# Optimization experiments

Hardware: AMD Instinct MI355X
Metric: run time of the kernel (lower is better)

## Reference

```python
import jax, jax.numpy as jnp
import numpy as np

N_ROI = 262144
FEATURE_DIM = 256
HIDDEN_DIM = 64
N_NETWORKS = 128


def setup_inputs() -> dict:
    key = jax.random.key(0)
    ks = jax.random.split(key, 5)
    x = jax.random.normal(ks[0], (N_ROI, FEATURE_DIM), dtype=jnp.float32)
    group = jax.random.randint(ks[1], (N_ROI,), 0, N_NETWORKS, dtype=jnp.int32)
    W1 = jax.random.normal(ks[2], (FEATURE_DIM, HIDDEN_DIM), dtype=jnp.float32) / np.sqrt(FEATURE_DIM)
    b1 = jnp.zeros((HIDDEN_DIM,), dtype=jnp.float32)
    W2 = jax.random.normal(ks[3], (HIDDEN_DIM, 1), dtype=jnp.float32) / np.sqrt(HIDDEN_DIM)
    b2 = jnp.zeros((1,), dtype=jnp.float32)
    return {"x": x, "group": group, "W1": W1, "b1": b1, "W2": W2, "b2": b2}


def reference(x, group, W1, b1, W2, b2):
    # attention MLP score per ROI: Linear -> ReLU -> Linear(->1)
    h = jax.nn.relu(x @ W1 + b1)                       # [N, H]
    score = (h @ W2)[:, 0] + b2[0]                     # [N]
    # numerically-stable segment softmax over each network's ROIs
    seg_max = jax.ops.segment_max(score, group, num_segments=N_NETWORKS)  # [K]
    seg_max = jnp.where(jnp.isfinite(seg_max), seg_max, 0.0)              # empty segments -> 0
    w = jnp.exp(score - seg_max[group])                # [N] unnormalized weights
    denom = jax.ops.segment_sum(w, group, num_segments=N_NETWORKS)        # [K]
    num = jax.ops.segment_sum(w[:, None] * x, group, num_segments=N_NETWORKS)  # [K, D]
    # empty networks produce zeros (matches torch.zeros_like branch)
    return jnp.where(denom[:, None] > 0, num / jnp.maximum(denom, 1e-30)[:, None], 0.0)
```

## Files before the change

kernel.cpp:

```cpp
#include <hip/hip_runtime.h>
#include <hip/hip_bf16.h>

#define N_ROI 262144
#define FDIM  256
#define HDIM  64
#define NNET  128

#define CHUNK  64
#define NCHUNK 16
#define RPB    (CHUNK * NCHUNK)
#define NBLK   (N_ROI / RPB)
#define XPITCH 264
#define WPITCH 264
#define APITCH 72
#define STRIP  40.0f

typedef __attribute__((ext_vector_type(8))) __bf16 bf16x8;
typedef __attribute__((ext_vector_type(8))) short short8;
typedef __attribute__((ext_vector_type(4))) float floatx4;

union frag_cast { short8 s; bf16x8 b; };

#define NEG_INF (-__builtin_huge_valf())

__device__ __forceinline__ unsigned fkey(float f) {
  unsigned u = __float_as_uint(f);
  return (u & 0x80000000u) ? ~u : (u | 0x80000000u);
}
__device__ __forceinline__ float fkey_inv(unsigned k) {
  unsigned u = (k & 0x80000000u) ? (k ^ 0x80000000u) : ~k;
  return __uint_as_float(u);
}
__device__ __forceinline__ unsigned short f2bf(float f) {
  unsigned u = __float_as_uint(f);
  u += 0x7FFFu + ((u >> 16) & 1u);
  return (unsigned short)(u >> 16);
}
__device__ __forceinline__ float bf2f(unsigned short h) {
  return __uint_as_float(((unsigned)h) << 16);
}
__device__ __forceinline__ unsigned cvt2(float a, float b) {
  union { __hip_bfloat162 h; unsigned u; } cv;
  cv.h = __float22bfloat162_rn(make_float2(a, b));
  return cv.u;
}
__device__ __forceinline__ int sidx(int row, int s) {
  return row * XPITCH + (s ^ (((row >> 3) & 3) << 4));
}

__device__ __forceinline__ void block_bar() {
  __builtin_amdgcn_sched_barrier(0);
  asm volatile("s_waitcnt lgkmcnt(0)" ::: "memory");
  __builtin_amdgcn_s_barrier();
  __builtin_amdgcn_sched_barrier(0);
}

__global__ __launch_bounds__(1024, 4) void fused_kernel(
    const float* __restrict__ x, const int* __restrict__ group,
    const float* __restrict__ W1, const float* __restrict__ b1,
    const float* __restrict__ W2,
    float* __restrict__ num_ws,
    float* __restrict__ den_ws,
    float* __restrict__ m_ws)
{
  __shared__ __align__(16) unsigned short w1t[HDIM][WPITCH];
  __shared__ __align__(16) unsigned short xl[2][CHUNK * XPITCH];
  __shared__ __align__(16) unsigned short Alds[2][NNET * APITCH];
  __shared__ float scpart[4][CHUNK];
  __shared__ unsigned tmax[NNET];
  __shared__ __align__(16) float fl[NNET];
  __shared__ float mrunL[NNET];
  __shared__ float dent[2][NNET];
  __shared__ int sflag[2];

  const int tid  = threadIdx.x;
  const int wave = tid >> 6, lane = tid & 63;
  const int col  = lane & 15, quad = lane >> 4;
  const int h    = wave >> 2;
  const int mt   = wave & 3;
  const int bid  = blockIdx.x;
  const size_t rbase = (size_t)bid * RPB;

  {
    const int n = tid & 63, kg = tid >> 6;
#pragma unroll
    for (int p = 0; p < 2; ++p) {
      const int k0 = (p * 16 + kg) * 8;
      unsigned short tmp[8];
#pragma unroll
      for (int j = 0; j < 8; ++j) tmp[j] = f2bf(W1[(k0 + j) * HDIM + n]);
      *(short8*)&w1t[n][k0] = *(short8*)tmp;
    }
  }
  if (tid < NNET) { mrunL[tid] = 0.f; dent[1][tid] = 0.f; }
  if (tid == 0) sflag[1] = 0;
  float denrun = 0.f;

  const float b1s = b1[h * 16 + col];
  const float w2s = W2[h * 16 + col];

  floatx4 acc[8];
#pragma unroll
  for (int m2 = 0; m2 < 8; ++m2) acc[m2] = (floatx4)0.f;

  const float* xb = x + rbase * FDIM;
  const short8 zero8 = (short8)0;

  float4 pf[4];
#pragma unroll
  for (int i = 0; i < 4; ++i) pf[i] = *(const float4*)(xb + i * 4096 + tid * 4);
#pragma unroll
  for (int i = 0; i < 4; ++i) {
    const int row = i * 16 + wave;
    uint2 pk; pk.x = cvt2(pf[i].x, pf[i].y); pk.y = cvt2(pf[i].z, pf[i].w);
    *(uint2*)&xl[0][sidx(row, (tid & 63) * 4)] = pk;
  }
#pragma unroll
  for (int i = 0; i < 4; ++i)
    pf[i] = *(const float4*)(xb + 16384 + i * 4096 + tid * 4);
  block_bar();

  int gch = 0;
  for (int ch = 0; ch < NCHUNK; ++ch) {
    const int b = ch & 1;

    if (sflag[b ^ 1]) {
#pragma unroll
      for (int m2 = 0; m2 < 8; ++m2) {
        const floatx4 f4 = *(const floatx4*)&fl[m2 * 16 + quad * 4];
#pragma unroll
        for (int r = 0; r < 4; ++r) acc[m2][r] *= f4[r];
      }
      if (tid < NNET) denrun *= fl[tid];
    }
    if (tid < NNET) denrun += dent[b ^ 1][tid];

    if (tid < CHUNK) gch = group[rbase + ch * CHUNK + tid];
    for (int k8 = tid; k8 < (NNET * APITCH) / 8; k8 += 1024)
      *(short8*)&Alds[b][k8 * 8] = zero8;
    if (tid < NNET) { tmax[tid] = 0u; dent[b][tid] = 0.f; }
    if (tid == 0) sflag[b] = 0;

    floatx4 accS = (floatx4)0.f;
#pragma unroll
    for (int c = 0; c < 8; ++c) {
      frag_cast af, bw;
      af.s = *(const short8*)&xl[b][sidx(mt * 16 + col, c * 32 + quad * 8)];
      bw.s = *(const short8*)&w1t[h * 16 + col][c * 32 + quad * 8];
      accS = __builtin_amdgcn_mfma_f32_16x16x32_bf16(af.b, bw.b, accS, 0, 0, 0);
    }
    {
      float pr[4];
#pragma unroll
      for (int r = 0; r < 4; ++r) pr[r] = fmaxf(accS[r] + b1s, 0.f) * w2s;
#pragma unroll
      for (int off = 1; off < 16; off <<= 1)
#pragma unroll
        for (int r = 0; r < 4; ++r) pr[r] += __shfl_xor(pr[r], off, 16);
      if (col == 0) {
#pragma unroll
        for (int r = 0; r < 4; ++r) scpart[h][mt * 16 + quad * 4 + r] = pr[r];
      }
    }

    if (ch > 0) {
#pragma unroll
      for (int cc = 0; cc < 2; ++cc) {
        frag_cast bfx;
        {
          unsigned short bb[8];
#pragma unroll
          for (int j = 0; j < 8; ++j)
            bb[j] = xl[b ^ 1][sidx(cc * 32 + quad * 8 + j, wave * 16 + col)];
          bfx.s = *(short8*)bb;
        }
#pragma unroll
        for (int m2 = 0; m2 < 8; ++m2) {
          frag_cast af;
          af.s = *(const short8*)&Alds[b ^ 1][(m2 * 16 + col) * APITCH + cc * 32 + quad * 8];
          acc[m2] = __builtin_amdgcn_mfma_f32_16x16x32_bf16(af.b, bfx.b, acc[m2], 0, 0, 0);
        }
      }
    }
    block_bar();

    if (tid < CHUNK) {
      const float s = scpart[0][tid] + scpart[1][tid] + scpart[2][tid] + scpart[3][tid];
      const float m = mrunL[gch];
      const bool trip = !(s - m <= STRIP);
      const unsigned long long bal = __ballot(trip);
      if (bal == 0ull) {
        const float w = __expf(s - m);
        const unsigned short wb = f2bf(w);
        Alds[b][gch * APITCH + tid] = wb;
        atomicAdd(&dent[b][gch], bf2f(wb));
      } else {
        atomicMax(&tmax[gch], fkey(s));
        asm volatile("s_waitcnt lgkmcnt(0)" ::: "memory");
#pragma unroll
        for (int hh = 0; hh < 2; ++hh) {
          const int gi = tid + hh * 64;
          const unsigned tk = tmax[gi];
          float f = 1.f;
          float mo = mrunL[gi];
          if (tk) {
            const float mn = fmaxf(mo, fkey_inv(tk));
            f = __expf(mo - mn);
            mo = mn;
            mrunL[gi] = mn;
          }
          fl[gi] = f;
        }
        asm volatile("s_waitcnt lgkmcnt(0)" ::: "memory");
        {
          const float w = __expf(s - mrunL[gch]);
          const unsigned short wb = f2bf(w);
          Alds[b][gch * APITCH + tid] = wb;
          atomicAdd(&dent[b][gch], bf2f(wb));
        }
        if (tid == 0) sflag[b] = 1;
      }
    }
    if (ch < NCHUNK - 1) {
#pragma unroll
      for (int i = 0; i < 4; ++i) {
        const int row = i * 16 + wave;
        uint2 pk; pk.x = cvt2(pf[i].x, pf[i].y); pk.y = cvt2(pf[i].z, pf[i].w);
        *(uint2*)&xl[b ^ 1][sidx(row, (tid & 63) * 4)] = pk;
      }
      if (ch < NCHUNK - 2) {
#pragma unroll
        for (int i = 0; i < 4; ++i)
          pf[i] = *(const float4*)(xb + (size_t)(ch + 2) * 16384 + i * 4096 + tid * 4);
      }
    }
    block_bar();
  }

  {
    const int b = (NCHUNK - 1) & 1;
    if (sflag[b]) {
#pragma unroll
      for (int m2 = 0; m2 < 8; ++m2) {
        const floatx4 f4 = *(const floatx4*)&fl[m2 * 16 + quad * 4];
#pragma unroll
        for (int r = 0; r < 4; ++r) acc[m2][r] *= f4[r];
      }
      if (tid < NNET) denrun *= fl[tid];
    }
    if (tid < NNET) denrun += dent[b][tid];
#pragma unroll
    for (int cc = 0; cc < 2; ++cc) {
      frag_cast bfx;
      {
        unsigned short bb[8];
#pragma unroll
        for (int j = 0; j < 8; ++j)
          bb[j] = xl[b][sidx(cc * 32 + quad * 8 + j, wave * 16 + col)];
        bfx.s = *(short8*)bb;
      }
#pragma unroll
      for (int m2 = 0; m2 < 8; ++m2) {
        frag_cast af;
        af.s = *(const short8*)&Alds[b][(m2 * 16 + col) * APITCH + cc * 32 + quad * 8];
        acc[m2] = __builtin_amdgcn_mfma_f32_16x16x32_bf16(af.b, bfx.b, acc[m2], 0, 0, 0);
      }
    }
  }

#pragma unroll
  for (int m2 = 0; m2 < 8; ++m2)
#pragma unroll
    for (int r = 0; r < 4; ++r) {
      const int g = m2 * 16 + quad * 4 + r;
      num_ws[((size_t)g * NBLK + bid) * FDIM + wave * 16 + col] = acc[m2][r];
    }
  if (tid < NNET) {
    den_ws[(size_t)tid * NBLK + bid] = denrun;
    m_ws[(size_t)tid * NBLK + bid]   = mrunL[tid];
  }
}

__global__ __launch_bounds__(256) void finalize_kernel(
    const float* __restrict__ num_ws, const float* __restrict__ den_ws,
    const float* __restrict__ m_ws, float* __restrict__ out)
{
  const int g   = blockIdx.x;
  const int tid = threadIdx.x;
  __shared__ float e_l[NBLK];
  __shared__ float red[8];

  const float mb = m_ws[(size_t)g * NBLK + tid];
  float M = mb;
#pragma unroll
  for (int off = 1; off < 64; off <<= 1) M = fmaxf(M, __shfl_xor(M, off));
  if ((tid & 63) == 0) red[tid >> 6] = M;
  __syncthreads();
  M = fmaxf(fmaxf(red[0], red[1]), fmaxf(red[2], red[3]));

  const float eb = (mb == NEG_INF) ? 0.f : __expf(mb - M);
  e_l[tid] = eb;
  float dp = den_ws[(size_t)g * NBLK + tid] * eb;
#pragma unroll
  for (int off = 1; off < 64; off <<= 1) dp += __shfl_xor(dp, off);
  if ((tid & 63) == 0) red[4 + (tid >> 6)] = dp;
  __syncthreads();
  const float den = red[4] + red[5] + red[6] + red[7];

  float nsum = 0.f;
  const float* base = num_ws + (size_t)g * NBLK * FDIM + tid;
#pragma unroll 8
  for (int b = 0; b < NBLK; ++b)
    nsum += base[(size_t)b * FDIM] * e_l[b];
  out[g * FDIM + tid] = (den > 0.f) ? nsum / fmaxf(den, 1e-30f) : 0.f;
}

extern "C" void kernel_launch(void* const* d_in, const int* in_sizes, int n_in,
                              void* d_out, int out_size, void* d_ws, size_t ws_size,
                              hipStream_t stream)
{
  const float* x     = (const float*)d_in[0];
  const int*   group = (const int*)d_in[1];
  const float* W1    = (const float*)d_in[2];
  const float* b1    = (const float*)d_in[3];
  const float* W2    = (const float*)d_in[4];
  float* out = (float*)d_out;

  float* num_ws = (float*)d_ws;
  float* den_ws = num_ws + (size_t)NNET * NBLK * FDIM;
  float* m_ws   = den_ws + (size_t)NNET * NBLK;

  fused_kernel<<<NBLK, 1024, 0, stream>>>(x, group, W1, b1, W2, num_ws, den_ws, m_ws);
  finalize_kernel<<<NNET, 256, 0, stream>>>(num_ws, den_ws, m_ws, out);

  (void)in_sizes; (void)n_in; (void)out_size; (void)ws_size;
}
```

Measured before the change: 380.9 us.

## Specialize waves into score and scatter groups with single sparsely-cleared A buffer

Waves 0-7 now compute only the score GEMM, two row tiles each. Waves 8-15 own the weighted-scatter accumulation, two feature tiles each, with accumulators doubled per wave. The double-buffered one-hot weight matrix becomes a single buffer: instead of zeroing it every chunk, only the entries written in the previous chunk are cleared. An XOR swizzle is added to the W1 and weight-matrix LDS layouts to cut bank conflicts. The goal is to drop the full per-chunk LDS zeroing and to overlap the two GEMM phases across SIMDs. In exchange, the wave groups now carry unequal MFMA loads, and the scatter waves need more registers.

Result: slower. 440.6 us (+15.7%).

```diff
diff --git a/kernel.cpp b/kernel.cpp
--- a/kernel.cpp
+++ b/kernel.cpp
@@ -46,6 +46,9 @@
 }
 __device__ __forceinline__ int sidx(int row, int s) {
   return row * XPITCH + (s ^ (((row >> 3) & 3) << 4));
+}
+__device__ __forceinline__ int cswz(int row, int k) {
+  return k ^ ((row & 3) << 4);
 }
 
 __device__ __forceinline__ void block_bar() {
@@ -65,7 +68,7 @@
 {
   __shared__ __align__(16) unsigned short w1t[HDIM][WPITCH];
   __shared__ __align__(16) unsigned short xl[2][CHUNK * XPITCH];
-  __shared__ __align__(16) unsigned short Alds[2][NNET * APITCH];
+  __shared__ __align__(16) unsigned short Alds[NNET * APITCH];
   __shared__ float scpart[4][CHUNK];
   __shared__ unsigned tmax[NNET];
   __shared__ __align__(16) float fl[NNET];
@@ -76,8 +79,10 @@
   const int tid  = threadIdx.x;
   const int wave = tid >> 6, lane = tid & 63;
   const int col  = lane & 15, quad = lane >> 4;
-  const int h    = wave >> 2;
-  const int mt   = wave & 3;
+  const bool is_scat = (wave >= 8);
+  const int d8   = wave & 7;
+  const int h    = (wave >> 1) & 3;
+  const int mt0  = (wave & 1) * 2;
   const int bid  = blockIdx.x;
   const size_t rbase = (size_t)bid * RPB;
 
@@ -89,22 +94,24 @@
       unsigned short tmp[8];
 #pragma unroll
       for (int j = 0; j < 8; ++j) tmp[j] = f2bf(W1[(k0 + j) * HDIM + n]);
-      *(short8*)&w1t[n][k0] = *(short8*)tmp;
+      *(short8*)&w1t[n][cswz(n, k0)] = *(short8*)tmp;
     }
   }
   if (tid < NNET) { mrunL[tid] = 0.f; dent[1][tid] = 0.f; }
   if (tid == 0) sflag[1] = 0;
+  const short8 zero8 = (short8)0;
+  for (int k8 = tid; k8 < (NNET * APITCH) / 8; k8 += 1024)
+    *(short8*)&Alds[k8 * 8] = zero8;
   float denrun = 0.f;
 
   const float b1s = b1[h * 16 + col];
   const float w2s = W2[h * 16 + col];
 
-  floatx4 acc[8];
-#pragma unroll
-  for (int m2 = 0; m2 < 8; ++m2) acc[m2] = (floatx4)0.f;
+  floatx4 acc[8][2];
+#pragma unroll
+  for (int m2 = 0; m2 < 8; ++m2) { acc[m2][0] = (floatx4)0.f; acc[m2][1] = (floatx4)0.f; }
 
   const float* xb = x + rbase * FDIM;
-  const short8 zero8 = (short8)0;
 
   float4 pf[4];
 #pragma unroll
@@ -120,65 +127,76 @@
     pf[i] = *(const float4*)(xb + 16384 + i * 4096 + tid * 4);
   block_bar();
 
-  int gch = 0;
+  int gch = 0, gprev = 0;
   for (int ch = 0; ch < NCHUNK; ++ch) {
     const int b = ch & 1;
 
-    if (sflag[b ^ 1]) {
-#pragma unroll
-      for (int m2 = 0; m2 < 8; ++m2) {
-        const floatx4 f4 = *(const floatx4*)&fl[m2 * 16 + quad * 4];
-#pragma unroll
-        for (int r = 0; r < 4; ++r) acc[m2][r] *= f4[r];
-      }
-      if (tid < NNET) denrun *= fl[tid];
-    }
-    if (tid < NNET) denrun += dent[b ^ 1][tid];
-
+    if (tid < NNET) {
+      if (sflag[b ^ 1]) denrun *= fl[tid];
+      denrun += dent[b ^ 1][tid];
+      tmax[tid] = 0u; dent[b][tid] = 0.f;
+    }
+    if (tid == 0) sflag[b] = 0;
     if (tid < CHUNK) gch = group[rbase + ch * CHUNK + tid];
-    for (int k8 = tid; k8 < (NNET * APITCH) / 8; k8 += 1024)
-      *(short8*)&Alds[b][k8 * 8] = zero8;
-    if (tid < NNET) { tmax[tid] = 0u; dent[b][tid] = 0.f; }
-    if (tid == 0) sflag[b] = 0;
-
-    floatx4 accS = (floatx4)0.f;
-#pragma unroll
-    for (int c = 0; c < 8; ++c) {
-      frag_cast af, bw;
-      af.s = *(const short8*)&xl[b][sidx(mt * 16 + col, c * 32 + quad * 8)];
-      bw.s = *(const short8*)&w1t[h * 16 + col][c * 32 + quad * 8];
-      accS = __builtin_amdgcn_mfma_f32_16x16x32_bf16(af.b, bw.b, accS, 0, 0, 0);
-    }
-    {
-      float pr[4];
-#pragma unroll
-      for (int r = 0; r < 4; ++r) pr[r] = fmaxf(accS[r] + b1s, 0.f) * w2s;
-#pragma unroll
-      for (int off = 1; off < 16; off <<= 1)
-#pragma unroll
-        for (int r = 0; r < 4; ++r) pr[r] += __shfl_xor(pr[r], off, 16);
-      if (col == 0) {
-#pragma unroll
-        for (int r = 0; r < 4; ++r) scpart[h][mt * 16 + quad * 4 + r] = pr[r];
-      }
-    }
-
-    if (ch > 0) {
-#pragma unroll
-      for (int cc = 0; cc < 2; ++cc) {
-        frag_cast bfx;
-        {
-          unsigned short bb[8];
-#pragma unroll
-          for (int j = 0; j < 8; ++j)
-            bb[j] = xl[b ^ 1][sidx(cc * 32 + quad * 8 + j, wave * 16 + col)];
-          bfx.s = *(short8*)bb;
-        }
+
+    if (!is_scat) {
+      floatx4 accS[2];
+      accS[0] = (floatx4)0.f; accS[1] = (floatx4)0.f;
+#pragma unroll
+      for (int c = 0; c < 8; ++c) {
+        frag_cast bw;
+        bw.s = *(const short8*)&w1t[h * 16 + col][cswz(col, c * 32 + quad * 8)];
+#pragma unroll
+        for (int mtl = 0; mtl < 2; ++mtl) {
+          frag_cast af;
+          af.s = *(const short8*)&xl[b][sidx((mt0 + mtl) * 16 + col, c * 32 + quad * 8)];
+          accS[mtl] = __builtin_amdgcn_mfma_f32_16x16x32_bf16(af.b, bw.b, accS[mtl], 0, 0, 0);
+        }
+      }
+#pragma unroll
+      for (int mtl = 0; mtl < 2; ++mtl) {
+        float pr[4];
+#pragma unroll
+        for (int r = 0; r < 4; ++r) pr[r] = fmaxf(accS[mtl][r] + b1s, 0.f) * w2s;
+#pragma unroll
+        for (int off = 1; off < 16; off <<= 1)
+#pragma unroll
+          for (int r = 0; r < 4; ++r) pr[r] += __shfl_xor(pr[r], off, 16);
+        if (col == 0) {
+#pragma unroll
+          for (int r = 0; r < 4; ++r)
+            scpart[h][(mt0 + mtl) * 16 + quad * 4 + r] = pr[r];
+        }
+      }
+    } else {
+      if (sflag[b ^ 1]) {
 #pragma unroll
         for (int m2 = 0; m2 < 8; ++m2) {
-          frag_cast af;
-          af.s = *(const short8*)&Alds[b ^ 1][(m2 * 16 + col) * APITCH + cc * 32 + quad * 8];
-          acc[m2] = __builtin_amdgcn_mfma_f32_16x16x32_bf16(af.b, bfx.b, acc[m2], 0, 0, 0);
+          const floatx4 f4 = *(const floatx4*)&fl[m2 * 16 + quad * 4];
+#pragma unroll
+          for (int r = 0; r < 4; ++r) { acc[m2][0][r] *= f4[r]; acc[m2][1][r] *= f4[r]; }
+        }
+      }
+      if (ch > 0) {
+#pragma unroll
+        for (int cc = 0; cc < 2; ++cc) {
+          frag_cast bfx[2];
+#pragma unroll
+          for (int nt = 0; nt < 2; ++nt) {
+            unsigned short bb[8];
+#pragma unroll
+            for (int j = 0; j < 8; ++j)
+              bb[j] = xl[b ^ 1][sidx(cc * 32 + quad * 8 + j, d8 * 32 + nt * 16 + col)];
+            bfx[nt].s = *(short8*)bb;
+          }
+#pragma unroll
+          for (int m2 = 0; m2 < 8; ++m2) {
+            frag_cast af;
+            af.s = *(const short8*)&Alds[(m2 * 16 + col) * APITCH
+                                         + cswz(col, cc * 32 + quad * 8)];
+            acc[m2][0] = __builtin_amdgcn_mfma_f32_16x16x32_bf16(af.b, bfx[0].b, acc[m2][0], 0, 0, 0);
+            acc[m2][1] = __builtin_amdgcn_mfma_f32_16x16x32_bf16(af.b, bfx[1].b, acc[m2][1], 0, 0, 0);
+          }
         }
       }
     }
@@ -186,13 +204,14 @@
 
     if (tid < CHUNK) {
       const float s = scpart[0][tid] + scpart[1][tid] + scpart[2][tid] + scpart[3][tid];
+      Alds[gprev * APITCH + (tid ^ ((gprev & 3) << 4))] = 0;
       const float m = mrunL[gch];
       const bool trip = !(s - m <= STRIP);
       const unsigned long long bal = __ballot(trip);
       if (bal == 0ull) {
         const float w = __expf(s - m);
         const unsigned short wb = f2bf(w);
-        Alds[b][gch * APITCH + tid] = wb;
+        Alds[gch * APITCH + (tid ^ ((gch & 3) << 4))] = wb;
         atomicAdd(&dent[b][gch], bf2f(wb));
       } else {
         atomicMax(&tmax[gch], fkey(s));
@@ -202,11 +221,10 @@
           const int gi = tid + hh * 64;
           const unsigned tk = tmax[gi];
           float f = 1.f;
-          float mo = mrunL[gi];
           if (tk) {
+            const float mo = mrunL[gi];
             const float mn = fmaxf(mo, fkey_inv(tk));
             f = __expf(mo - mn);
-            mo = mn;
             mrunL[gi] = mn;
           }
           fl[gi] = f;
@@ -215,11 +233,12 @@
         {
           const float w = __expf(s - mrunL[gch]);
           const unsigned short wb = f2bf(w);
-          Alds[b][gch * APITCH + tid] = wb;
+          Alds[gch * APITCH + (tid ^ ((gch & 3) << 4))] = wb;
           atomicAdd(&dent[b][gch], bf2f(wb));
         }
         if (tid == 0) sflag[b] = 1;
       }
+      gprev = gch;
     }
     if (ch < NCHUNK - 1) {
 #pragma unroll
@@ -239,42 +258,53 @@
 
   {
     const int b = (NCHUNK - 1) & 1;
-    if (sflag[b]) {
-#pragma unroll
-      for (int m2 = 0; m2 < 8; ++m2) {
-        const floatx4 f4 = *(const floatx4*)&fl[m2 * 16 + quad * 4];
-#pragma unroll
-        for (int r = 0; r < 4; ++r) acc[m2][r] *= f4[r];
-      }
-      if (tid < NNET) denrun *= fl[tid];
-    }
-    if (tid < NNET) denrun += dent[b][tid];
-#pragma unroll
-    for (int cc = 0; cc < 2; ++cc) {
-      frag_cast bfx;
-      {
-        unsigned short bb[8];
-#pragma unroll
-        for (int j = 0; j < 8; ++j)
-          bb[j] = xl[b][sidx(cc * 32 + quad * 8 + j, wave * 16 + col)];
-        bfx.s = *(short8*)bb;
-      }
-#pragma unroll
-      for (int m2 = 0; m2 < 8; ++m2) {
-        frag_cast af;
-        af.s = *(const short8*)&Alds[b][(m2 * 16 + col) * APITCH + cc * 32 + quad * 8];
-        acc[m2] = __builtin_amdgcn_mfma_f32_16x16x32_bf16(af.b, bfx.b, acc[m2], 0, 0, 0);
-      }
-    }
-  }
-
-#pragma unroll
-  for (int m2 = 0; m2 < 8; ++m2)
-#pragma unroll
-    for (int r = 0; r < 4; ++r) {
-      const int g = m2 * 16 + quad * 4 + r;
-      num_ws[((size_t)g * NBLK + bid) * FDIM + wave * 16 + col] = acc[m2][r];
-    }
+    if (tid < NNET) {
+      if (sflag[b]) denrun *= fl[tid];
+      denrun += dent[b][tid];
+    }
+    if (is_scat) {
+      if (sflag[b]) {
+#pragma unroll
+        for (int m2 = 0; m2 < 8; ++m2) {
+          const floatx4 f4 = *(const floatx4*)&fl[m2 * 16 + quad * 4];
+#pragma unroll
+          for (int r = 0; r < 4; ++r) { acc[m2][0][r] *= f4[r]; acc[m2][1][r] *= f4[r]; }
+        }
+      }
+#pragma unroll
+      for (int cc = 0; cc < 2; ++cc) {
+        frag_cast bfx[2];
+#pragma unroll
+        for (int nt = 0; nt < 2; ++nt) {
+          unsigned short bb[8];
+#pragma unroll
+          for (int j = 0; j < 8; ++j)
+            bb[j] = xl[b][sidx(cc * 32 + quad * 8 + j, d8 * 32 + nt * 16 + col)];
+          bfx[nt].s = *(short8*)bb;
+        }
+#pragma unroll
+        for (int m2 = 0; m2 < 8; ++m2) {
+          frag_cast af;
+          af.s = *(const short8*)&Alds[(m2 * 16 + col) * APITCH
+                                       + cswz(col, cc * 32 + quad * 8)];
+          acc[m2][0] = __builtin_amdgcn_mfma_f32_16x16x32_bf16(af.b, bfx[0].b, acc[m2][0], 0, 0, 0);
+          acc[m2][1] = __builtin_amdgcn_mfma_f32_16x16x32_bf16(af.b, bfx[1].b, acc[m2][1], 0, 0, 0);
+        }
+      }
+    }
+  }
+
+  if (is_scat) {
+#pragma unroll
+    for (int m2 = 0; m2 < 8; ++m2)
+#pragma unroll
+      for (int nt = 0; nt < 2; ++nt)
+#pragma unroll
+        for (int r = 0; r < 4; ++r) {
+          const int g = m2 * 16 + quad * 4 + r;
+          num_ws[((size_t)g * NBLK + bid) * FDIM + d8 * 32 + nt * 16 + col] = acc[m2][nt][r];
+        }
+  }
   if (tid < NNET) {
     den_ws[(size_t)tid * NBLK + bid] = denrun;
     m_ws[(size_t)tid * NBLK + bid]   = mrunL[tid];
```

## Build one-hot A fragments in registers from packed group/weight pairs; keep W1 in registers

Applied to the files above, without the earlier changes.

Replaces the zero-filled dense [NNET x CHUNK] bf16 weight matrix in LDS with a compact per-row packed (group<<16 | bf16 weight) array. Each lane builds the one-hot A fragment for the segment-sum MFMA with compare/select in registers. W1 fragments are also preloaded into registers instead of being staged in LDS, and the den bookkeeping is reordered. This removes the per-chunk LDS zeroing and dense A loads and cuts LDS footprint, at the cost of extra VALU select work and register pressure under launch_bounds(1024,4).

Measured after the change: 517.3 us. +35.8%, slower.

```diff
diff --git a/kernel.cpp b/kernel.cpp
--- a/kernel.cpp
+++ b/kernel.cpp
@@ -11,8 +11,6 @@
 #define RPB    (CHUNK * NCHUNK)
 #define NBLK   (N_ROI / RPB)
 #define XPITCH 264
-#define WPITCH 264
-#define APITCH 72
 #define STRIP  40.0f
 
 typedef __attribute__((ext_vector_type(8))) __bf16 bf16x8;
@@ -63,9 +61,8 @@
     float* __restrict__ den_ws,
     float* __restrict__ m_ws)
 {
-  __shared__ __align__(16) unsigned short w1t[HDIM][WPITCH];
   __shared__ __align__(16) unsigned short xl[2][CHUNK * XPITCH];
-  __shared__ __align__(16) unsigned short Alds[2][NNET * APITCH];
+  __shared__ __align__(16) unsigned gwlds[2][CHUNK];
   __shared__ float scpart[4][CHUNK];
   __shared__ unsigned tmax[NNET];
   __shared__ __align__(16) float fl[NNET];
@@ -81,30 +78,27 @@
   const int bid  = blockIdx.x;
   const size_t rbase = (size_t)bid * RPB;
 
-  {
-    const int n = tid & 63, kg = tid >> 6;
-#pragma unroll
-    for (int p = 0; p < 2; ++p) {
-      const int k0 = (p * 16 + kg) * 8;
-      unsigned short tmp[8];
-#pragma unroll
-      for (int j = 0; j < 8; ++j) tmp[j] = f2bf(W1[(k0 + j) * HDIM + n]);
-      *(short8*)&w1t[n][k0] = *(short8*)tmp;
-    }
-  }
+  frag_cast w1f[8];
+#pragma unroll
+  for (int c = 0; c < 8; ++c) {
+    unsigned short tmp[8];
+#pragma unroll
+    for (int j = 0; j < 8; ++j)
+      tmp[j] = f2bf(W1[(c * 32 + quad * 8 + j) * HDIM + h * 16 + col]);
+    w1f[c].s = *(short8*)tmp;
+  }
+  const float b1s = b1[h * 16 + col];
+  const float w2s = W2[h * 16 + col];
+
   if (tid < NNET) { mrunL[tid] = 0.f; dent[1][tid] = 0.f; }
   if (tid == 0) sflag[1] = 0;
   float denrun = 0.f;
 
-  const float b1s = b1[h * 16 + col];
-  const float w2s = W2[h * 16 + col];
-
   floatx4 acc[8];
 #pragma unroll
   for (int m2 = 0; m2 < 8; ++m2) acc[m2] = (floatx4)0.f;
 
   const float* xb = x + rbase * FDIM;
-  const short8 zero8 = (short8)0;
 
   float4 pf[4];
 #pragma unroll
@@ -124,6 +118,35 @@
   for (int ch = 0; ch < NCHUNK; ++ch) {
     const int b = ch & 1;
 
+    if (tid < NNET) {
+      if (sflag[b ^ 1]) denrun *= fl[tid];
+      denrun += dent[b ^ 1][tid];
+      tmax[tid] = 0u; dent[b][tid] = 0.f;
+    }
+    if (tid == 0) sflag[b] = 0;
+    if (tid < CHUNK) gch = group[rbase + ch * CHUNK + tid];
+
+    floatx4 accS = (floatx4)0.f;
+#pragma unroll
+    for (int c = 0; c < 8; ++c) {
+      frag_cast af;
+      af.s = *(const short8*)&xl[b][sidx(mt * 16 + col, c * 32 + quad * 8)];
+      accS = __builtin_amdgcn_mfma_f32_16x16x32_bf16(af.b, w1f[c].b, accS, 0, 0, 0);
+    }
+    {
+      float pr[4];
+#pragma unroll
+      for (int r = 0; r < 4; ++r) pr[r] = fmaxf(accS[r] + b1s, 0.f) * w2s;
+#pragma unroll
+      for (int off = 1; off < 16; off <<= 1)
+#pragma unroll
+        for (int r = 0; r < 4; ++r) pr[r] += __shfl_xor(pr[r], off, 16);
+      if (col == 0) {
+#pragma unroll
+        for (int r = 0; r < 4; ++r) scpart[h][mt * 16 + quad * 4 + r] = pr[r];
+      }
+    }
+
     if (sflag[b ^ 1]) {
 #pragma unroll
       for (int m2 = 0; m2 < 8; ++m2) {
@@ -131,39 +154,13 @@
 #pragma unroll
         for (int r = 0; r < 4; ++r) acc[m2][r] *= f4[r];
       }
-      if (tid < NNET) denrun *= fl[tid];
-    }
-    if (tid < NNET) denrun += dent[b ^ 1][tid];
-
-    if (tid < CHUNK) gch = group[rbase + ch * CHUNK + tid];
-    for (int k8 = tid; k8 < (NNET * APITCH) / 8; k8 += 1024)
-      *(short8*)&Alds[b][k8 * 8] = zero8;
-    if (tid < NNET) { tmax[tid] = 0u; dent[b][tid] = 0.f; }
-    if (tid == 0) sflag[b] = 0;
-
-    floatx4 accS = (floatx4)0.f;
-#pragma unroll
-    for (int c = 0; c < 8; ++c) {
-      frag_cast af, bw;
-      af.s = *(const short8*)&xl[b][sidx(mt * 16 + col, c * 32 + quad * 8)];
-      bw.s = *(const short8*)&w1t[h * 16 + col][c * 32 + quad * 8];
-      accS = __builtin_amdgcn_mfma_f32_16x16x32_bf16(af.b, bw.b, accS, 0, 0, 0);
-    }
-    {
-      float pr[4];
-#pragma unroll
-      for (int r = 0; r < 4; ++r) pr[r] = fmaxf(accS[r] + b1s, 0.f) * w2s;
-#pragma unroll
-      for (int off = 1; off < 16; off <<= 1)
-#pragma unroll
-        for (int r = 0; r < 4; ++r) pr[r] += __shfl_xor(pr[r], off, 16);
-      if (col == 0) {
-#pragma unroll
-        for (int r = 0; r < 4; ++r) scpart[h][mt * 16 + quad * 4 + r] = pr[r];
-      }
-    }
-
+    }
     if (ch > 0) {
+      unsigned gwv[16];
+      *(uint4*)&gwv[0]  = *(const uint4*)&gwlds[b ^ 1][quad * 8];
+      *(uint4*)&gwv[4]  = *(const uint4*)&gwlds[b ^ 1][quad * 8 + 4];
+      *(uint4*)&gwv[8]  = *(const uint4*)&gwlds[b ^ 1][32 + quad * 8];
+      *(uint4*)&gwv[12] = *(const uint4*)&gwlds[b ^ 1][32 + quad * 8 + 4];
 #pragma unroll
       for (int cc = 0; cc < 2; ++cc) {
         frag_cast bfx;
@@ -176,8 +173,14 @@
         }
 #pragma unroll
         for (int m2 = 0; m2 < 8; ++m2) {
-          frag_cast af;
-          af.s = *(const short8*)&Alds[b ^ 1][(m2 * 16 + col) * APITCH + cc * 32 + quad * 8];
+          const unsigned gt = (unsigned)(m2 * 16 + col);
+          unsigned short aa[8];
+#pragma unroll
+          for (int j = 0; j < 8; ++j) {
+            const unsigned g2 = gwv[cc * 8 + j];
+            aa[j] = ((g2 >> 16) == gt) ? (unsigned short)g2 : (unsigned short)0;
+          }
+          frag_cast af; af.s = *(short8*)aa;
           acc[m2] = __builtin_amdgcn_mfma_f32_16x16x32_bf16(af.b, bfx.b, acc[m2], 0, 0, 0);
         }
       }
@@ -192,7 +195,7 @@
       if (bal == 0ull) {
         const float w = __expf(s - m);
         const unsigned short wb = f2bf(w);
-        Alds[b][gch * APITCH + tid] = wb;
+        gwlds[b][tid] = ((unsigned)gch << 16) | wb;
         atomicAdd(&dent[b][gch], bf2f(wb));
       } else {
         atomicMax(&tmax[gch], fkey(s));
@@ -202,11 +205,10 @@
           const int gi = tid + hh * 64;
           const unsigned tk = tmax[gi];
           float f = 1.f;
-          float mo = mrunL[gi];
           if (tk) {
+            const float mo = mrunL[gi];
             const float mn = fmaxf(mo, fkey_inv(tk));
             f = __expf(mo - mn);
-            mo = mn;
             mrunL[gi] = mn;
           }
           fl[gi] = f;
@@ -215,7 +217,7 @@
         {
           const float w = __expf(s - mrunL[gch]);
           const unsigned short wb = f2bf(w);
-          Alds[b][gch * APITCH + tid] = wb;
+          gwlds[b][tid] = ((unsigned)gch << 16) | wb;
           atomicAdd(&dent[b][gch], bf2f(wb));
         }
         if (tid == 0) sflag[b] = 1;
@@ -239,6 +241,10 @@
 
   {
     const int b = (NCHUNK - 1) & 1;
+    if (tid < NNET) {
+      if (sflag[b]) denrun *= fl[tid];
+      denrun += dent[b][tid];
+    }
     if (sflag[b]) {
 #pragma unroll
       for (int m2 = 0; m2 < 8; ++m2) {
@@ -246,9 +252,12 @@
 #pragma unroll
         for (int r = 0; r < 4; ++r) acc[m2][r] *= f4[r];
       }
-      if (tid < NNET) denrun *= fl[tid];
-    }
-    if (tid < NNET) denrun += dent[b][tid];
+    }
+    unsigned gwv[16];
+    *(uint4*)&gwv[0]  = *(const uint4*)&gwlds[b][quad * 8];
+    *(uint4*)&gwv[4]  = *(const uint4*)&gwlds[b][quad * 8 + 4];
+    *(uint4*)&gwv[8]  = *(const uint4*)&gwlds[b][32 + quad * 8];
+    *(uint4*)&gwv[12] = *(const uint4*)&gwlds[b][32 + quad * 8 + 4];
 #pragma unroll
     for (int cc = 0; cc < 2; ++cc) {
       frag_cast bfx;
@@ -261,8 +270,14 @@
       }
 #pragma unroll
       for (int m2 = 0; m2 < 8; ++m2) {
-        frag_cast af;
-        af.s = *(const short8*)&Alds[b][(m2 * 16 + col) * APITCH + cc * 32 + quad * 8];
+        const unsigned gt = (unsigned)(m2 * 16 + col);
+        unsigned short aa[8];
+#pragma unroll
+        for (int j = 0; j < 8; ++j) {
+          const unsigned g2 = gwv[cc * 8 + j];
+          aa[j] = ((g2 >> 16) == gt) ? (unsigned short)g2 : (unsigned short)0;
+        }
+        frag_cast af; af.s = *(short8*)aa;
         acc[m2] = __builtin_amdgcn_mfma_f32_16x16x32_bf16(af.b, bfx.b, acc[m2], 0, 0, 0);
       }
     }
```
